# Kernel tuning notes

Measured on AMD Instinct MI355X. Metric: run time of the kernel, lower is better.

## Reference

```python
import jax, jax.numpy as jnp
import numpy as np

C = 256
G = 32            # GroupNorm groups = min(32, C)
DQK = C // 8      # q/k channel dim
EPS = 1e-5


def setup_inputs() -> dict:
    key = jax.random.key(0)
    ks = jax.random.split(key, 10)
    B, H, W = 4, 64, 64
    s = 0.02
    return {
        "x": jax.random.normal(ks[0], (B, C, H, W), dtype=jnp.float32),
        "gamma": jnp.ones((C,), jnp.float32),
        "beta": jnp.zeros((C,), jnp.float32),
        "wq": jax.random.normal(ks[1], (DQK, C), jnp.float32) * s,
        "bq": jnp.zeros((DQK,), jnp.float32),
        "wk": jax.random.normal(ks[2], (DQK, C), jnp.float32) * s,
        "bk": jnp.zeros((DQK,), jnp.float32),
        "wv": jax.random.normal(ks[3], (C, C), jnp.float32) * s,
        "bv": jnp.zeros((C,), jnp.float32),
        "wp": jax.random.normal(ks[4], (C, C), jnp.float32) * s,
        "bp": jnpp if False else jnp.zeros((C,), jnp.float32),
    }


def reference(x, gamma, beta, wq, bq, wk, bk, wv, bv, wp, bp):
    B, Cc, H, W = x.shape
    N = H * W
    # GroupNorm(32, C), affine
    h = x.reshape(B, G, Cc // G, H, W)
    mu = h.mean(axis=(2, 3, 4), keepdims=True)
    var = h.var(axis=(2, 3, 4), keepdims=True)
    h = (h - mu) * jax.lax.rsqrt(var + EPS)
    h = h.reshape(B, Cc, N) * gamma[:, None] + beta[:, None]
    # 1x1 convs == per-token linear maps over channels
    q = jnp.einsum('dc,bcn->bnd', wq, h) + bq            # [B, N, DQK]
    k = jnp.einsum('dc,bcn->bdn', wk, h) + bk[:, None]   # [B, DQK, N]
    v = jnp.einsum('ec,bcn->ben', wv, h) + bv[:, None]   # [B, C, N]
    scale = DQK ** (-0.5)
    attn = jax.nn.softmax(jnp.einsum('bnd,bdm->bnm', q, k) * scale, axis=-1)
    out = jnp.einsum('bnm,bem->ben', attn, v)            # [B, C, N]
    proj = jnp.einsum('fe,ben->bfn', wp, out) + bp[:, None]
    return x + proj.reshape(B, Cc, H, W)
```

## Files before the change

### kernel.cpp

```cpp
#include <hip/hip_runtime.h>
#include <hip/hip_bf16.h>

#define NB 4
#define CD 256
#define NT 4096
#define DQ 32

typedef __attribute__((ext_vector_type(8))) __bf16 bf16x8;
typedef __attribute__((ext_vector_type(16))) float float16v;
typedef __attribute__((ext_vector_type(4))) unsigned int uint4v;
typedef __attribute__((ext_vector_type(2))) unsigned int uint2v;

#if __has_builtin(__builtin_amdgcn_exp2f)
#define EXP2(x) __builtin_amdgcn_exp2f(x)
#else
#define EXP2(x) exp2f(x)
#endif

__device__ inline unsigned short f2bf(float f) {
  unsigned u = __float_as_uint(f);
  u += 0x7fffu + ((u >> 16) & 1u);
  return (unsigned short)(u >> 16);
}

__global__ __launch_bounds__(256) void gn_prep(
    const float* __restrict__ x, float* __restrict__ accum,
    const float* __restrict__ wq, const float* __restrict__ wk,
    const float* __restrict__ wv, const float* __restrict__ wp,
    const float* __restrict__ bq, const float* __restrict__ bk,
    const float* __restrict__ bv, unsigned short* __restrict__ wqkv,
    unsigned short* __restrict__ wpb, float* __restrict__ bias) {
  int bx = blockIdx.x;
  int tid = threadIdx.x;
  if (bx < 512) {
    int bg = bx >> 2, ch = bx & 3;
    const float4* xp = (const float4*)(x + (size_t)bg * 32768 + ch * 8192);
    float s = 0.f, ss = 0.f;
#pragma unroll
    for (int i = 0; i < 8; i++) {
      float4 v = xp[tid + 256 * i];
      s += v.x + v.y + v.z + v.w;
      ss += v.x * v.x + v.y * v.y + v.z * v.z + v.w * v.w;
    }
    int wid = tid >> 6, lane = tid & 63;
#pragma unroll
    for (int off = 32; off >= 1; off >>= 1) {
      s += __shfl_xor(s, off);
      ss += __shfl_xor(ss, off);
    }
    __shared__ float red[8];
    if (lane == 0) { red[wid] = s; red[4 + wid] = ss; }
    __syncthreads();
    if (tid == 0) {
      accum[2 * bx] = red[0] + red[1] + red[2] + red[3];
      accum[2 * bx + 1] = red[4] + red[5] + red[6] + red[7];
    }
  } else {
    const float scale2 = 0.2550348909867343f;
    int i = (bx - 512) * 256 + tid;
    if (i < 320 * 256) {
      int j = i >> 8, c = i & 255;
      float v;
      if (j < 32) v = wq[j * 256 + c] * scale2;
      else if (j < 64) v = wk[(j - 32) * 256 + c];
      else v = wv[(j - 64) * 256 + c];
      wqkv[i] = f2bf(v);
    } else if (i < 320 * 256 + 256 * 256) {
      int k = i - 320 * 256;
      wpb[k] = f2bf(wp[k]);
    } else if (i < 320 * 256 + 256 * 256 + 320) {
      int j = i - (320 * 256 + 256 * 256);
      float v;
      if (j < 32) v = bq[j] * scale2;
      else if (j < 64) v = bk[j - 32];
      else v = bv[j - 64];
      bias[j] = v;
    }
  }
}

__global__ __launch_bounds__(256) void gn_apply(
    const float* __restrict__ x, const float* __restrict__ gamma,
    const float* __restrict__ beta, const float* __restrict__ accum,
    unsigned short* __restrict__ h) {
  int bg = blockIdx.x >> 2, nc = blockIdx.x & 3;
  int tid = threadIdx.x;
  float S = accum[8 * bg] + accum[8 * bg + 2] + accum[8 * bg + 4] +
            accum[8 * bg + 6];
  float SS = accum[8 * bg + 1] + accum[8 * bg + 3] + accum[8 * bg + 5] +
             accum[8 * bg + 7];
  float mu = S * (1.f / 32768.f);
  float var = SS * (1.f / 32768.f) - mu * mu;
  float rstd = rsqrtf(var + 1e-5f);
  int b = bg >> 5, g = bg & 31, c0 = g * 8;
  float gam[8], bet[8];
#pragma unroll
  for (int j = 0; j < 8; j++) { gam[j] = gamma[c0 + j]; bet[j] = beta[c0 + j]; }
  const float* xb = x + (size_t)bg * 32768;
#pragma unroll
  for (int i = 0; i < 4; i++) {
    int n = nc * 1024 + tid + 256 * i;
    unsigned short hv[8];
#pragma unroll
    for (int j = 0; j < 8; j++) {
      float y = (xb[j * NT + n] - mu) * rstd * gam[j] + bet[j];
      hv[j] = f2bf(y);
    }
    *(uint4v*)(h + ((size_t)(b * NT + n) * CD + c0)) = *(uint4v*)hv;
  }
}

__global__ __launch_bounds__(256) void qkv_gemm(
    const unsigned short* __restrict__ A, const unsigned short* __restrict__ H,
    const float* __restrict__ bias, unsigned short* __restrict__ qk,
    unsigned short* __restrict__ v) {
  int nt = blockIdx.x, mt = blockIdx.y, b = blockIdx.z;
  int tid = threadIdx.x, lane = tid & 63;
  int w = tid >> 6, mi = w & 1, ni = w >> 1;
  int l31 = lane & 31, hh = lane >> 5;
  int m_base = mt * 64 + 32 * mi;
  int n_base = nt * 128 + 64 * ni;
  const unsigned short* Arow = A + (size_t)(m_base + l31) * 256 + 8 * hh;
  const unsigned short* Hb = H + (size_t)b * NT * CD;
  const unsigned short* h0 = Hb + (size_t)(n_base + l31) * CD + 8 * hh;
  const unsigned short* h1 = h0 + (size_t)32 * CD;
  float16v acc0, acc1;
#pragma unroll
  for (int r = 0; r < 16; r++) { acc0[r] = 0.f; acc1[r] = 0.f; }
#pragma unroll
  for (int s = 0; s < 16; s++) {
    bf16x8 af = *(const bf16x8*)(Arow + 16 * s);
    bf16x8 b0 = *(const bf16x8*)(h0 + 16 * s);
    bf16x8 b1 = *(const bf16x8*)(h1 + 16 * s);
    acc0 = __builtin_amdgcn_mfma_f32_32x32x16_bf16(af, b0, acc0, 0, 0, 0);
    acc1 = __builtin_amdgcn_mfma_f32_32x32x16_bf16(af, b1, acc1, 0, 0, 0);
  }
  float bj[16];
  int jr[16];
#pragma unroll
  for (int r = 0; r < 16; r++) {
    jr[r] = m_base + (r & 3) + 8 * (r >> 2) + 4 * hh;
    bj[r] = bias[jr[r]];
  }
#pragma unroll
  for (int half = 0; half < 2; half++) {
    int n = n_base + 32 * half + l31;
#pragma unroll
    for (int r = 0; r < 16; r++) {
      float val = (half ? acc1[r] : acc0[r]) + bj[r];
      int j = jr[r];
      if (j < 64) {
        qk[((size_t)b * NT + n) * 64 + j] = f2bf(val);
      } else {
        v[((size_t)b * CD + (j - 64)) * NT + n] = f2bf(val);
      }
    }
  }
}

__global__ __launch_bounds__(512, 4) void attn_fused(
    const unsigned short* __restrict__ qk, const unsigned short* __restrict__ V,
    unsigned short* __restrict__ Pa, unsigned short* __restrict__ Pb,
    float* __restrict__ lp4) {
  int L = blockIdx.x;
  int xv = L & 7;
  int b = xv >> 1;
  int kh = xv & 1;
  int n0 = (L >> 3) * 64;
  int tid = threadIdx.x, lane = tid & 63, w = tid >> 6;
  int qi = w & 1, kj = (w >> 1) & 1, eo = w >> 2;
  int l31 = lane & 31, hh = lane >> 5;

  __shared__ unsigned short Ks[64 * 36];
  __shared__ unsigned short Vs[256 * 68];
  __shared__ unsigned short Pbuf[2 * 32 * 68];

  const unsigned short* qkb = qk + (size_t)b * NT * 64;
  const unsigned short* Vb = V + (size_t)b * CD * NT;

  int n_g = n0 + 32 * qi + l31;
  bf16x8 qfr[2];
  qfr[0] = *(const bf16x8*)&qkb[(size_t)n_g * 64 + 8 * hh];
  qfr[1] = *(const bf16x8*)&qkb[(size_t)n_g * 64 + 8 * hh + 16];

  int se = tid >> 1, smh = (tid & 1) * 32;
  int skr = tid >> 2, skc = (tid & 3) * 8;

  int mbase = kh * 2048;
  uint4v vreg[4];
  uint4v kreg;
  {
    const unsigned short* vp = &Vb[(size_t)se * NT + mbase + smh];
#pragma unroll
    for (int u = 0; u < 4; u++) vreg[u] = *(const uint4v*)(vp + 8 * u);
    if (tid < 256)
      kreg = *(const uint4v*)&qkb[(size_t)(mbase + skr) * 64 + 32 + skc];
  }

  float16v acc[2];
#pragma unroll
  for (int et = 0; et < 2; et++)
#pragma unroll
    for (int r = 0; r < 16; r++) acc[et][r] = 0.f;
  float lsum = 0.f;
  unsigned short* Prow = &Pbuf[(qi * 32 + l31) * 68];

  for (int it = 0; it < 32; it++) {
    if (tid < 256) {
      *(uint4v*)&Ks[skr * 36 + skc] = kreg;
      if (it + 1 < 32) {
        int m1 = mbase + (it + 1) * 64;
        kreg = *(const uint4v*)&qkb[(size_t)(m1 + skr) * 64 + 32 + skc];
      }
    }
    __syncthreads();

#pragma unroll
    for (int u = 0; u < 4; u++)
      *(uint4v*)&Vs[se * 68 + smh + 8 * u] = vreg[u];
    if (it + 1 < 32) {
      int m1 = mbase + (it + 1) * 64;
      const unsigned short* vp = &Vb[(size_t)se * NT + m1 + smh];
#pragma unroll
      for (int u = 0; u < 4; u++) vreg[u] = *(const uint4v*)(vp + 8 * u);
    }

    if (eo == 0) {
      float16v st;
#pragma unroll
      for (int r = 0; r < 16; r++) st[r] = 0.f;
#pragma unroll
      for (int s = 0; s < 2; s++) {
        bf16x8 af = *(const bf16x8*)&Ks[(32 * kj + l31) * 36 + 16 * s + 8 * hh];
        st = __builtin_amdgcn_mfma_f32_32x32x16_bf16(af, qfr[s], st, 0, 0, 0);
      }
#pragma unroll
      for (int rq = 0; rq < 4; rq++) {
        float e0 = EXP2(st[4 * rq + 0]);
        float e1 = EXP2(st[4 * rq + 1]);
        float e2 = EXP2(st[4 * rq + 2]);
        float e3 = EXP2(st[4 * rq + 3]);
        lsum += (e0 + e1) + (e2 + e3);
        uint2v pw;
        pw[0] = __builtin_amdgcn_perm(__float_as_uint(e1), __float_as_uint(e0),
                                      0x07060302u);
        pw[1] = __builtin_amdgcn_perm(__float_as_uint(e3), __float_as_uint(e2),
                                      0x07060302u);
        *(uint2v*)&Prow[8 * rq + 4 * hh + 32 * kj] = pw;
      }
    }
    __syncthreads();

#pragma unroll
    for (int sp = 0; sp < 4; sp++) {
      bf16x8 afr =
          *(const bf16x8*)&Pbuf[(qi * 32 + l31) * 68 + 16 * sp + 8 * hh];
#pragma unroll
      for (int et = 0; et < 2; et++) {
        int etile = 4 * eo + 2 * kj + et;
        bf16x8 bfr =
            *(const bf16x8*)&Vs[(32 * etile + l31) * 68 + 16 * sp + 8 * hh];
        acc[et] =
            __builtin_amdgcn_mfma_f32_32x32x16_bf16(afr, bfr, acc[et], 0, 0, 0);
      }
    }
  }

  if (eo == 0) {
    lsum += __shfl_xor(lsum, 32);
    if (hh == 0) {
      lp4[(size_t)((kh * 2 + kj) * NB + b) * NT + n0 + 32 * qi + l31] = lsum;
    }
  }
  unsigned short* Pout = (kh ? Pb : Pa) + (size_t)b * NT * CD;
#pragma unroll
  for (int r = 0; r < 16; r++) {
    int nl = (r & 3) + 8 * (r >> 2) + 4 * hh;
    size_t row = (size_t)(n0 + 32 * qi + nl) * CD + l31;
#pragma unroll
    for (int et = 0; et < 2; et++) {
      int etile = 4 * eo + 2 * kj + et;
      Pout[row + 32 * etile] = f2bf(acc[et][r]);
    }
  }
}

__device__ inline bf16x8 combine_frag(const unsigned short* p0,
                                      const unsigned short* p1, float inv) {
  uint4v ua = *(const uint4v*)p0;
  uint4v ub = *(const uint4v*)p1;
  uint4v r;
#pragma unroll
  for (int j = 0; j < 4; j++) {
    float lo = __uint_as_float(ua[j] << 16) + __uint_as_float(ub[j] << 16);
    float hi = __uint_as_float(ua[j] & 0xffff0000u) +
               __uint_as_float(ub[j] & 0xffff0000u);
    lo *= inv;
    hi *= inv;
    r[j] = __builtin_amdgcn_perm(__float_as_uint(hi), __float_as_uint(lo),
                                 0x07060302u);
  }
  return *(bf16x8*)&r;
}

__global__ __launch_bounds__(256) void proj_gemm(
    const unsigned short* __restrict__ Wp, const unsigned short* __restrict__ Pa,
    const unsigned short* __restrict__ Pb, const float* __restrict__ lp4,
    const float* __restrict__ bp, const float* __restrict__ x,
    float* __restrict__ out) {
  int nt = blockIdx.x, mt = blockIdx.y, b = blockIdx.z;
  int tid = threadIdx.x, lane = tid & 63;
  int w = tid >> 6, mi = w & 1, ni = w >> 1;
  int l31 = lane & 31, hh = lane >> 5;
  int m_base = mt * 64 + 32 * mi;
  int n_base = nt * 128 + 64 * ni;
  const unsigned short* Arow = Wp + (size_t)(m_base + l31) * 256 + 8 * hh;
  int nA = n_base + l31, nB = nA + 32;
  float lA = 0.f, lB = 0.f;
#pragma unroll
  for (int s4 = 0; s4 < 4; s4++) {
    lA += lp4[(size_t)(s4 * NB + b) * NT + nA];
    lB += lp4[(size_t)(s4 * NB + b) * NT + nB];
  }
  float invA = 1.f / lA, invB = 1.f / lB;
  const unsigned short* a0 = Pa + ((size_t)b * NT + nA) * CD + 8 * hh;
  const unsigned short* a1 = Pa + ((size_t)b * NT + nB) * CD + 8 * hh;
  const unsigned short* c0 = Pb + ((size_t)b * NT + nA) * CD + 8 * hh;
  const unsigned short* c1 = Pb + ((size_t)b * NT + nB) * CD + 8 * hh;
  float16v acc0, acc1;
#pragma unroll
  for (int r = 0; r < 16; r++) { acc0[r] = 0.f; acc1[r] = 0.f; }
#pragma unroll
  for (int s = 0; s < 16; s++) {
    bf16x8 af = *(const bf16x8*)(Arow + 16 * s);
    bf16x8 b0 = combine_frag(a0 + 16 * s, c0 + 16 * s, invA);
    bf16x8 b1 = combine_frag(a1 + 16 * s, c1 + 16 * s, invB);
    acc0 = __builtin_amdgcn_mfma_f32_32x32x16_bf16(af, b0, acc0, 0, 0, 0);
    acc1 = __builtin_amdgcn_mfma_f32_32x32x16_bf16(af, b1, acc1, 0, 0, 0);
  }
#pragma unroll
  for (int half = 0; half < 2; half++) {
    int n = n_base + 32 * half + l31;
#pragma unroll
    for (int r = 0; r < 16; r++) {
      int f = m_base + (r & 3) + 8 * (r >> 2) + 4 * hh;
      size_t idx = ((size_t)b * CD + f) * NT + n;
      out[idx] = x[idx] + (half ? acc1[r] : acc0[r]) + bp[f];
    }
  }
}

extern "C" void kernel_launch(void* const* d_in, const int* in_sizes, int n_in,
                              void* d_out, int out_size, void* d_ws,
                              size_t ws_size, hipStream_t stream) {
  (void)in_sizes; (void)n_in; (void)out_size; (void)ws_size;
  const float* x = (const float*)d_in[0];
  const float* gamma = (const float*)d_in[1];
  const float* beta = (const float*)d_in[2];
  const float* wq = (const float*)d_in[3];
  const float* bq = (const float*)d_in[4];
  const float* wk = (const float*)d_in[5];
  const float* bk = (const float*)d_in[6];
  const float* wv = (const float*)d_in[7];
  const float* bv = (const float*)d_in[8];
  const float* wp = (const float*)d_in[9];
  const float* bp = (const float*)d_in[10];
  float* out = (float*)d_out;

  char* ws = (char*)d_ws;
  unsigned short* h_ws = (unsigned short*)ws;
  unsigned short* qk_ws = (unsigned short*)(ws + 8388608);
  unsigned short* v_ws = (unsigned short*)(ws + 10485760);
  unsigned short* o_ws = (unsigned short*)(ws + 18874368);
  unsigned short* wqkv_b = (unsigned short*)(ws + 27262976);
  unsigned short* wp_b = (unsigned short*)(ws + 27426816);
  float* bias_q = (float*)(ws + 27557888);
  float* accum = (float*)(ws + 27559168);
  float* lp4 = (float*)(ws + 27563264);

  gn_prep<<<1090, 256, 0, stream>>>(x, accum, wq, wk, wv, wp, bq, bk, bv,
                                    wqkv_b, wp_b, bias_q);
  gn_apply<<<512, 256, 0, stream>>>(x, gamma, beta, accum, h_ws);
  dim3 gq(32, 5, NB);
  qkv_gemm<<<gq, 256, 0, stream>>>(wqkv_b, h_ws, bias_q, qk_ws, v_ws);
  attn_fused<<<512, 512, 0, stream>>>(qk_ws, v_ws, h_ws, o_ws, lp4);
  dim3 gp(32, 4, NB);
  proj_gemm<<<gp, 256, 0, stream>>>(wp_b, h_ws, o_ws, lp4, bp, x, out);
}
```

Baseline: 193.7 us.

## Pre-swizzle V into MFMA fragment layout and load it directly from global

```diff
diff --git a/kernel.cpp b/kernel.cpp
--- a/kernel.cpp
+++ b/kernel.cpp
@@ -152,14 +152,19 @@
       if (j < 64) {
         qk[((size_t)b * NT + n) * 64 + j] = f2bf(val);
       } else {
-        v[((size_t)b * CD + (j - 64)) * NT + n] = f2bf(val);
+        int e = j - 64;
+        int itg = n >> 6, sp = (n >> 4) & 3;
+        int ls = ((n >> 3) & 1) * 32 + (e & 31);
+        int el = n & 7, et = e >> 5;
+        v[((((size_t)b * 64 + itg) * 8 + et) * 4 + sp) * 512 + ls * 8 + el] =
+            f2bf(val);
       }
     }
   }
 }
 
 __global__ __launch_bounds__(512, 4) void attn_fused(
-    const unsigned short* __restrict__ qk, const unsigned short* __restrict__ V,
+    const unsigned short* __restrict__ qk, const unsigned short* __restrict__ Vp,
     unsigned short* __restrict__ Pa, unsigned short* __restrict__ Pb,
     float* __restrict__ lp4) {
   int L = blockIdx.x;
@@ -168,45 +173,49 @@
   int kh = xv & 1;
   int n0 = (L >> 3) * 64;
   int tid = threadIdx.x, lane = tid & 63, w = tid >> 6;
-  int qi = w & 1, kj = (w >> 1) & 1, eo = w >> 2;
   int l31 = lane & 31, hh = lane >> 5;
-
-  __shared__ unsigned short Ks[64 * 36];
-  __shared__ unsigned short Vs[256 * 68];
-  __shared__ unsigned short Pbuf[2 * 32 * 68];
+  int qs = w & 1, ks2 = (w >> 1) & 1;
+  int km = w & 1, grp = w >> 1;
+
+  __shared__ __align__(16) char smem[65536];
+  unsigned short* Ks = (unsigned short*)smem;
+  unsigned short* Pbuf = (unsigned short*)(smem + 4608);
+  float* red = (float*)smem;
 
   const unsigned short* qkb = qk + (size_t)b * NT * 64;
-  const unsigned short* Vb = V + (size_t)b * CD * NT;
-
-  int n_g = n0 + 32 * qi + l31;
+  const unsigned short* vit = Vp + ((size_t)b * 64 + kh * 32) * 16384;
+
+  int n_g = n0 + 32 * qs + l31;
   bf16x8 qfr[2];
   qfr[0] = *(const bf16x8*)&qkb[(size_t)n_g * 64 + 8 * hh];
   qfr[1] = *(const bf16x8*)&qkb[(size_t)n_g * 64 + 8 * hh + 16];
 
-  int se = tid >> 1, smh = (tid & 1) * 32;
-  int skr = tid >> 2, skc = (tid & 3) * 8;
-
+  int tK = tid - 256;
+  int skr = tK >> 2, skc = (tK & 3) * 8;
   int mbase = kh * 2048;
-  uint4v vreg[4];
   uint4v kreg;
-  {
-    const unsigned short* vp = &Vb[(size_t)se * NT + mbase + smh];
-#pragma unroll
-    for (int u = 0; u < 4; u++) vreg[u] = *(const uint4v*)(vp + 8 * u);
-    if (tid < 256)
-      kreg = *(const uint4v*)&qkb[(size_t)(mbase + skr) * 64 + 32 + skc];
-  }
-
-  float16v acc[2];
-#pragma unroll
-  for (int et = 0; et < 2; et++)
-#pragma unroll
-    for (int r = 0; r < 16; r++) acc[et][r] = 0.f;
+  if (tid >= 256)
+    kreg = *(const uint4v*)&qkb[(size_t)(mbase + skr) * 64 + 32 + skc];
+
+  float16v acc[2][2];
+#pragma unroll
+  for (int q2 = 0; q2 < 2; q2++)
+#pragma unroll
+    for (int e2 = 0; e2 < 2; e2++)
+#pragma unroll
+      for (int r = 0; r < 16; r++) acc[q2][e2][r] = 0.f;
   float lsum = 0.f;
-  unsigned short* Prow = &Pbuf[(qi * 32 + l31) * 68];
+  unsigned short* Prow = &Pbuf[(qs * 32 + l31) * 68];
 
   for (int it = 0; it < 32; it++) {
-    if (tid < 256) {
+    const unsigned short* vp0 =
+        vit + (size_t)it * 16384 + (grp * 8 + 2 * km) * 512 + lane * 8;
+    bf16x8 vf00 = *(const bf16x8*)(vp0);
+    bf16x8 vf01 = *(const bf16x8*)(vp0 + 512);
+    bf16x8 vf10 = *(const bf16x8*)(vp0 + 2048);
+    bf16x8 vf11 = *(const bf16x8*)(vp0 + 2560);
+
+    if (tid >= 256) {
       *(uint4v*)&Ks[skr * 36 + skc] = kreg;
       if (it + 1 < 32) {
         int m1 = mbase + (it + 1) * 64;
@@ -215,23 +224,13 @@
     }
     __syncthreads();
 
-#pragma unroll
-    for (int u = 0; u < 4; u++)
-      *(uint4v*)&Vs[se * 68 + smh + 8 * u] = vreg[u];
-    if (it + 1 < 32) {
-      int m1 = mbase + (it + 1) * 64;
-      const unsigned short* vp = &Vb[(size_t)se * NT + m1 + smh];
-#pragma unroll
-      for (int u = 0; u < 4; u++) vreg[u] = *(const uint4v*)(vp + 8 * u);
-    }
-
-    if (eo == 0) {
+    if (w < 4) {
       float16v st;
 #pragma unroll
       for (int r = 0; r < 16; r++) st[r] = 0.f;
 #pragma unroll
       for (int s = 0; s < 2; s++) {
-        bf16x8 af = *(const bf16x8*)&Ks[(32 * kj + l31) * 36 + 16 * s + 8 * hh];
+        bf16x8 af = *(const bf16x8*)&Ks[(32 * ks2 + l31) * 36 + 16 * s + 8 * hh];
         st = __builtin_amdgcn_mfma_f32_32x32x16_bf16(af, qfr[s], st, 0, 0, 0);
       }
 #pragma unroll
@@ -246,41 +245,80 @@
                                       0x07060302u);
         pw[1] = __builtin_amdgcn_perm(__float_as_uint(e3), __float_as_uint(e2),
                                       0x07060302u);
-        *(uint2v*)&Prow[8 * rq + 4 * hh + 32 * kj] = pw;
+        *(uint2v*)&Prow[8 * rq + 4 * hh + 32 * ks2] = pw;
       }
     }
     __syncthreads();
 
 #pragma unroll
-    for (int sp = 0; sp < 4; sp++) {
-      bf16x8 afr =
-          *(const bf16x8*)&Pbuf[(qi * 32 + l31) * 68 + 16 * sp + 8 * hh];
-#pragma unroll
-      for (int et = 0; et < 2; et++) {
-        int etile = 4 * eo + 2 * kj + et;
-        bf16x8 bfr =
-            *(const bf16x8*)&Vs[(32 * etile + l31) * 68 + 16 * sp + 8 * hh];
-        acc[et] =
-            __builtin_amdgcn_mfma_f32_32x32x16_bf16(afr, bfr, acc[et], 0, 0, 0);
-      }
-    }
-  }
-
-  if (eo == 0) {
+    for (int spL = 0; spL < 2; spL++) {
+      int sp = 2 * km + spL;
+      bf16x8 a0 = *(const bf16x8*)&Pbuf[(l31)*68 + 16 * sp + 8 * hh];
+      bf16x8 a1 = *(const bf16x8*)&Pbuf[(32 + l31) * 68 + 16 * sp + 8 * hh];
+      bf16x8 b0 = spL ? vf01 : vf00;
+      bf16x8 b1 = spL ? vf11 : vf10;
+      acc[0][0] = __builtin_amdgcn_mfma_f32_32x32x16_bf16(a0, b0, acc[0][0], 0, 0, 0);
+      acc[1][0] = __builtin_amdgcn_mfma_f32_32x32x16_bf16(a1, b0, acc[1][0], 0, 0, 0);
+      acc[0][1] = __builtin_amdgcn_mfma_f32_32x32x16_bf16(a0, b1, acc[0][1], 0, 0, 0);
+      acc[1][1] = __builtin_amdgcn_mfma_f32_32x32x16_bf16(a1, b1, acc[1][1], 0, 0, 0);
+    }
+  }
+
+  if (w < 4) {
     lsum += __shfl_xor(lsum, 32);
     if (hh == 0) {
-      lp4[(size_t)((kh * 2 + kj) * NB + b) * NT + n0 + 32 * qi + l31] = lsum;
-    }
-  }
+      lp4[(size_t)((kh * 2 + ks2) * NB + b) * NT + n0 + 32 * qs + l31] = lsum;
+    }
+  }
+
+  __syncthreads();
+  if (km == 0) {
+#pragma unroll
+    for (int e2 = 0; e2 < 2; e2++)
+#pragma unroll
+      for (int r = 0; r < 16; r++)
+        red[(w * 2 + e2) * 1024 + r * 64 + lane] = acc[1][e2][r];
+  } else {
+#pragma unroll
+    for (int e2 = 0; e2 < 2; e2++)
+#pragma unroll
+      for (int r = 0; r < 16; r++)
+        red[(w * 2 + e2) * 1024 + r * 64 + lane] = acc[0][e2][r];
+  }
+  __syncthreads();
+  int pw = w ^ 1;
+  if (km == 0) {
+#pragma unroll
+    for (int e2 = 0; e2 < 2; e2++)
+#pragma unroll
+      for (int r = 0; r < 16; r++)
+        acc[0][e2][r] += red[(pw * 2 + e2) * 1024 + r * 64 + lane];
+  } else {
+#pragma unroll
+    for (int e2 = 0; e2 < 2; e2++)
+#pragma unroll
+      for (int r = 0; r < 16; r++)
+        acc[1][e2][r] += red[(pw * 2 + e2) * 1024 + r * 64 + lane];
+  }
+
   unsigned short* Pout = (kh ? Pb : Pa) + (size_t)b * NT * CD;
-#pragma unroll
-  for (int r = 0; r < 16; r++) {
-    int nl = (r & 3) + 8 * (r >> 2) + 4 * hh;
-    size_t row = (size_t)(n0 + 32 * qi + nl) * CD + l31;
-#pragma unroll
-    for (int et = 0; et < 2; et++) {
-      int etile = 4 * eo + 2 * kj + et;
-      Pout[row + 32 * etile] = f2bf(acc[et][r]);
+  if (km == 0) {
+#pragma unroll
+    for (int r = 0; r < 16; r++) {
+      int nl = (r & 3) + 8 * (r >> 2) + 4 * hh;
+      size_t row = (size_t)(n0 + nl) * CD + l31;
+#pragma unroll
+      for (int e2 = 0; e2 < 2; e2++)
+        Pout[row + 32 * (2 * grp + e2)] = f2bf(acc[0][e2][r]);
+    }
+  } else {
+#pragma unroll
+    for (int r = 0; r < 16; r++) {
+      int nl = (r & 3) + 8 * (r >> 2) + 4 * hh;
+      size_t row = (size_t)(n0 + 32 + nl) * CD + l31;
+#pragma unroll
+      for (int e2 = 0; e2 < 2; e2++)
+        Pout[row + 32 * (2 * grp + e2)] = f2bf(acc[1][e2][r]);
     }
   }
 }
```

Result: slower. 233.2 us (+20.4%).

## Pre-swizzle V into MFMA fragment layout and software-pipeline QK/PV in attention

Applied to the files above, without the earlier changes.

```diff
diff --git a/kernel.cpp b/kernel.cpp
--- a/kernel.cpp
+++ b/kernel.cpp
@@ -22,6 +22,8 @@
   u += 0x7fffu + ((u >> 16) & 1u);
   return (unsigned short)(u >> 16);
 }
+
+#define BARRIER() asm volatile("s_waitcnt lgkmcnt(0)\n\ts_barrier" ::: "memory")
 
 __global__ __launch_bounds__(256) void gn_prep(
     const float* __restrict__ x, float* __restrict__ accum,
@@ -152,14 +154,73 @@
       if (j < 64) {
         qk[((size_t)b * NT + n) * 64 + j] = f2bf(val);
       } else {
-        v[((size_t)b * CD + (j - 64)) * NT + n] = f2bf(val);
+        int e = j - 64;
+        int itg = n >> 6, sp = (n >> 4) & 3;
+        int ls = ((n >> 3) & 1) * 32 + (e & 31);
+        int el = n & 7, et = e >> 5;
+        v[((((size_t)b * 64 + itg) * 8 + et) * 4 + sp) * 512 + ls * 8 + el] =
+            f2bf(val);
       }
     }
   }
 }
 
+#define K_STAGE(PCUR)                                                         \
+  if (tid >= 256) {                                                           \
+    *(uint4v*)&Ks[(((PCUR) + 1) & 1) * 2304 + skr * 36 + skc] = kreg;         \
+    int pk_ = (PCUR) + 2 <= 31 ? (PCUR) + 2 : 31;                             \
+    kreg =                                                                    \
+        *(const uint4v*)&qkb[(size_t)(mbase + pk_ * 64 + skr) * 64 + 32 + skc]; \
+  }
+
+#define QK_STEP(PCUR)                                                         \
+  if (w < 4) {                                                                \
+    float16v st;                                                              \
+    _Pragma("unroll") for (int r = 0; r < 16; r++) st[r] = 0.f;               \
+    _Pragma("unroll") for (int s = 0; s < 2; s++) {                           \
+      bf16x8 af = *(const bf16x8*)&Ks[((PCUR) & 1) * 2304 +                   \
+                                      (32 * ks2 + l31) * 36 + 16 * s + 8 * hh]; \
+      st = __builtin_amdgcn_mfma_f32_32x32x16_bf16(af, qfr[s], st, 0, 0, 0);  \
+    }                                                                         \
+    _Pragma("unroll") for (int rq = 0; rq < 4; rq++) {                        \
+      float e0 = EXP2(st[4 * rq + 0]);                                        \
+      float e1 = EXP2(st[4 * rq + 1]);                                        \
+      float e2 = EXP2(st[4 * rq + 2]);                                        \
+      float e3 = EXP2(st[4 * rq + 3]);                                        \
+      lsum += (e0 + e1) + (e2 + e3);                                          \
+      uint2v pw;                                                              \
+      pw[0] = __builtin_amdgcn_perm(__float_as_uint(e1), __float_as_uint(e0), \
+                                    0x07060302u);                             \
+      pw[1] = __builtin_amdgcn_perm(__float_as_uint(e3), __float_as_uint(e2), \
+                                    0x07060302u);                             \
+      *(uint2v*)&Pbuf[((PCUR) & 1) * 4352 + (qs * 32 + l31) * 68 + 8 * rq +   \
+                      4 * hh + 32 * ks2] = pw;                                \
+    }                                                                         \
+  }
+
+#define PV_STEP(PPREV, CURV)                                                  \
+  {                                                                           \
+    _Pragma("unroll") for (int sp = 0; sp < 4; sp++) {                        \
+      bf16x8 a0 = *(const bf16x8*)&Pbuf[((PPREV) & 1) * 4352 + l31 * 68 +     \
+                                        16 * sp + 8 * hh];                    \
+      bf16x8 a1 = *(const bf16x8*)&Pbuf[((PPREV) & 1) * 4352 +                \
+                                        (32 + l31) * 68 + 16 * sp + 8 * hh];  \
+      acc[0] = __builtin_amdgcn_mfma_f32_32x32x16_bf16(a0, CURV[sp], acc[0],  \
+                                                       0, 0, 0);              \
+      acc[1] = __builtin_amdgcn_mfma_f32_32x32x16_bf16(a1, CURV[sp], acc[1],  \
+                                                       0, 0, 0);              \
+    }                                                                         \
+  }
+
+#define V_LOAD(DST, ITX)                                                      \
+  {                                                                           \
+    const unsigned short* vp_ = vbase + (size_t)(ITX)*16384;                  \
+    _Pragma("unroll") for (int u = 0; u < 4; u++)                             \
+        DST[u] = *(const bf16x8*)(vp_ + u * 512);                             \
+  }
+
 __global__ __launch_bounds__(512, 4) void attn_fused(
-    const unsigned short* __restrict__ qk, const unsigned short* __restrict__ V,
+    const unsigned short* __restrict__ qk, const unsigned short* __restrict__ Vp,
     unsigned short* __restrict__ Pa, unsigned short* __restrict__ Pb,
     float* __restrict__ lp4) {
   int L = blockIdx.x;
@@ -168,120 +229,79 @@
   int kh = xv & 1;
   int n0 = (L >> 3) * 64;
   int tid = threadIdx.x, lane = tid & 63, w = tid >> 6;
-  int qi = w & 1, kj = (w >> 1) & 1, eo = w >> 2;
   int l31 = lane & 31, hh = lane >> 5;
-
-  __shared__ unsigned short Ks[64 * 36];
-  __shared__ unsigned short Vs[256 * 68];
-  __shared__ unsigned short Pbuf[2 * 32 * 68];
+  int qs = w & 1, ks2 = (w >> 1) & 1;
+
+  __shared__ unsigned short Ks[2 * 2304];
+  __shared__ unsigned short Pbuf[2 * 4352];
 
   const unsigned short* qkb = qk + (size_t)b * NT * 64;
-  const unsigned short* Vb = V + (size_t)b * CD * NT;
-
-  int n_g = n0 + 32 * qi + l31;
+  const unsigned short* vit = Vp + ((size_t)b * 64 + kh * 32) * 16384;
+  const unsigned short* vbase = vit + (size_t)w * 4 * 512 + lane * 8;
+
   bf16x8 qfr[2];
-  qfr[0] = *(const bf16x8*)&qkb[(size_t)n_g * 64 + 8 * hh];
-  qfr[1] = *(const bf16x8*)&qkb[(size_t)n_g * 64 + 8 * hh + 16];
-
-  int se = tid >> 1, smh = (tid & 1) * 32;
-  int skr = tid >> 2, skc = (tid & 3) * 8;
-
+  if (w < 4) {
+    int n_g = n0 + 32 * qs + l31;
+    qfr[0] = *(const bf16x8*)&qkb[(size_t)n_g * 64 + 8 * hh];
+    qfr[1] = *(const bf16x8*)&qkb[(size_t)n_g * 64 + 8 * hh + 16];
+  }
+
+  int tK = tid - 256;
+  int skr = tK >> 2, skc = (tK & 3) * 8;
   int mbase = kh * 2048;
-  uint4v vreg[4];
   uint4v kreg;
-  {
-    const unsigned short* vp = &Vb[(size_t)se * NT + mbase + smh];
-#pragma unroll
-    for (int u = 0; u < 4; u++) vreg[u] = *(const uint4v*)(vp + 8 * u);
-    if (tid < 256)
-      kreg = *(const uint4v*)&qkb[(size_t)(mbase + skr) * 64 + 32 + skc];
-  }
 
   float16v acc[2];
 #pragma unroll
-  for (int et = 0; et < 2; et++)
-#pragma unroll
-    for (int r = 0; r < 16; r++) acc[et][r] = 0.f;
+  for (int q2 = 0; q2 < 2; q2++)
+#pragma unroll
+    for (int r = 0; r < 16; r++) acc[q2][r] = 0.f;
   float lsum = 0.f;
-  unsigned short* Prow = &Pbuf[(qi * 32 + l31) * 68];
-
-  for (int it = 0; it < 32; it++) {
-    if (tid < 256) {
-      *(uint4v*)&Ks[skr * 36 + skc] = kreg;
-      if (it + 1 < 32) {
-        int m1 = mbase + (it + 1) * 64;
-        kreg = *(const uint4v*)&qkb[(size_t)(m1 + skr) * 64 + 32 + skc];
-      }
-    }
-    __syncthreads();
-
-#pragma unroll
-    for (int u = 0; u < 4; u++)
-      *(uint4v*)&Vs[se * 68 + smh + 8 * u] = vreg[u];
-    if (it + 1 < 32) {
-      int m1 = mbase + (it + 1) * 64;
-      const unsigned short* vp = &Vb[(size_t)se * NT + m1 + smh];
-#pragma unroll
-      for (int u = 0; u < 4; u++) vreg[u] = *(const uint4v*)(vp + 8 * u);
-    }
-
-    if (eo == 0) {
-      float16v st;
-#pragma unroll
-      for (int r = 0; r < 16; r++) st[r] = 0.f;
-#pragma unroll
-      for (int s = 0; s < 2; s++) {
-        bf16x8 af = *(const bf16x8*)&Ks[(32 * kj + l31) * 36 + 16 * s + 8 * hh];
-        st = __builtin_amdgcn_mfma_f32_32x32x16_bf16(af, qfr[s], st, 0, 0, 0);
-      }
-#pragma unroll
-      for (int rq = 0; rq < 4; rq++) {
-        float e0 = EXP2(st[4 * rq + 0]);
-        float e1 = EXP2(st[4 * rq + 1]);
-        float e2 = EXP2(st[4 * rq + 2]);
-        float e3 = EXP2(st[4 * rq + 3]);
-        lsum += (e0 + e1) + (e2 + e3);
-        uint2v pw;
-        pw[0] = __builtin_amdgcn_perm(__float_as_uint(e1), __float_as_uint(e0),
-                                      0x07060302u);
-        pw[1] = __builtin_amdgcn_perm(__float_as_uint(e3), __float_as_uint(e2),
-                                      0x07060302u);
-        *(uint2v*)&Prow[8 * rq + 4 * hh + 32 * kj] = pw;
-      }
-    }
-    __syncthreads();
-
-#pragma unroll
-    for (int sp = 0; sp < 4; sp++) {
-      bf16x8 afr =
-          *(const bf16x8*)&Pbuf[(qi * 32 + l31) * 68 + 16 * sp + 8 * hh];
-#pragma unroll
-      for (int et = 0; et < 2; et++) {
-        int etile = 4 * eo + 2 * kj + et;
-        bf16x8 bfr =
-            *(const bf16x8*)&Vs[(32 * etile + l31) * 68 + 16 * sp + 8 * hh];
-        acc[et] =
-            __builtin_amdgcn_mfma_f32_32x32x16_bf16(afr, bfr, acc[et], 0, 0, 0);
-      }
-    }
-  }
-
-  if (eo == 0) {
+
+  bf16x8 vA[4], vB[4];
+  V_LOAD(vA, 0);
+  if (tid >= 256) {
+    kreg = *(const uint4v*)&qkb[(size_t)(mbase + skr) * 64 + 32 + skc];
+    *(uint4v*)&Ks[skr * 36 + skc] = kreg;
+    kreg = *(const uint4v*)&qkb[(size_t)(mbase + 64 + skr) * 64 + 32 + skc];
+  }
+  BARRIER();
+
+  K_STAGE(0);
+  QK_STEP(0);
+  V_LOAD(vB, 1);
+  BARRIER();
+
+  for (int p = 1; p < 31; p += 2) {
+    K_STAGE(p);
+    QK_STEP(p);
+    PV_STEP(p - 1, vA);
+    V_LOAD(vA, p + 1);
+    BARRIER();
+    K_STAGE(p + 1);
+    QK_STEP(p + 1);
+    PV_STEP(p, vB);
+    V_LOAD(vB, p + 2);
+    BARRIER();
+  }
+  QK_STEP(31);
+  PV_STEP(30, vA);
+  BARRIER();
+  PV_STEP(31, vB);
+
+  if (w < 4) {
     lsum += __shfl_xor(lsum, 32);
     if (hh == 0) {
-      lp4[(size_t)((kh * 2 + kj) * NB + b) * NT + n0 + 32 * qi + l31] = lsum;
-    }
-  }
+      lp4[(size_t)((kh * 2 + ks2) * NB + b) * NT + n0 + 32 * qs + l31] = lsum;
+    }
+  }
+
   unsigned short* Pout = (kh ? Pb : Pa) + (size_t)b * NT * CD;
 #pragma unroll
   for (int r = 0; r < 16; r++) {
     int nl = (r & 3) + 8 * (r >> 2) + 4 * hh;
-    size_t row = (size_t)(n0 + 32 * qi + nl) * CD + l31;
-#pragma unroll
-    for (int et = 0; et < 2; et++) {
-      int etile = 4 * eo + 2 * kj + et;
-      Pout[row + 32 * etile] = f2bf(acc[et][r]);
-    }
+    Pout[(size_t)(n0 + nl) * CD + 32 * w + l31] = f2bf(acc[0][r]);
+    Pout[(size_t)(n0 + 32 + nl) * CD + 32 * w + l31] = f2bf(acc[1][r]);
   }
 }
 
```

New measurement: 186.1 us. -3.9%, faster.
